# Kernel tuning notes

Measured on AMD Instinct MI355X. Metric: run time of the kernel, lower is better.

Reference implementation:

```python
import jax, jax.numpy as jnp
import numpy as np

N, E, F_IN, E_DIM, H, G = 8192, 40960, 32, 8, 64, 64
EPS = 1e-5


def _lin(key, fan_in, fan_out):
    k1, k2 = jax.random.split(key)
    s = 1.0 / np.sqrt(fan_in)
    w = jax.random.uniform(k1, (fan_in, fan_out), jnp.float32, -s, s)
    b = jax.random.uniform(k2, (fan_out,), jnp.float32, -s, s)
    return w, b


def setup_inputs() -> dict:
    key = jax.random.key(0)
    ks = jax.random.split(key, 32)
    inp = {}
    inp['x'] = jax.random.normal(ks[0], (N, F_IN), jnp.float32)
    inp['edge_index'] = jax.random.randint(ks[1], (2, E), 0, N)
    inp['edge_attr'] = jax.random.normal(ks[2], (E, E_DIM), jnp.float32)
    inp['batch'] = jnp.sort(jax.random.randint(ks[3], (N,), 0, G))
    # NNConv 1 (F_IN -> H)
    inp['e1_w1'], inp['e1_b1'] = _lin(ks[4], E_DIM, H)
    inp['e1_w2'], inp['e1_b2'] = _lin(ks[5], H, F_IN * H)
    inp['root1_w'], inp['root1_b'] = _lin(ks[6], F_IN, H)
    inp['bn1_g'] = jnp.ones((H,), jnp.float32); inp['bn1_b'] = jnp.zeros((H,), jnp.float32)
    # NNConv 2 (H -> H)
    inp['e2_w1'], inp['e2_b1'] = _lin(ks[7], E_DIM, H)
    inp['e2_w2'], inp['e2_b2'] = _lin(ks[8], H, H * H)
    inp['root2_w'], inp['root2_b'] = _lin(ks[9], H, H)
    inp['bn2_g'] = jnp.ones((H,), jnp.float32); inp['bn2_b'] = jnp.zeros((H,), jnp.float32)
    # NNConv 3 (H -> H)
    inp['e3_w1'], inp['e3_b1'] = _lin(ks[10], E_DIM, H)
    inp['e3_w2'], inp['e3_b2'] = _lin(ks[11], H, H * H)
    inp['root3_w'], inp['root3_b'] = _lin(ks[12], H, H)
    inp['bn3_g'] = jnp.ones((H,), jnp.float32); inp['bn3_b'] = jnp.zeros((H,), jnp.float32)
    # attention gate MLP: H -> H//2 -> 1
    inp['gate_w1'], inp['gate_b1'] = _lin(ks[13], H, H // 2)
    inp['gate_w2'], inp['gate_b2'] = _lin(ks[14], H // 2, 1)
    # fc head: H -> 2H (BN, relu) -> H (BN, relu) -> 1
    inp['fc1_w'], inp['fc1_b'] = _lin(ks[15], H, 2 * H)
    inp['fcbn1_g'] = jnp.ones((2 * H,), jnp.float32); inp['fcbn1_b'] = jnp.zeros((2 * H,), jnp.float32)
    inp['fc2_w'], inp['fc2_b'] = _lin(ks[16], 2 * H, H)
    inp['fcbn2_g'] = jnp.ones((H,), jnp.float32); inp['fcbn2_b'] = jnp.zeros((H,), jnp.float32)
    inp['fc3_w'], inp['fc3_b'] = _lin(ks[17], H, 1)
    return inp


def _bn(x, g, b):
    # training-mode batch norm over node/graph dim
    m = jnp.mean(x, axis=0)
    v = jnp.var(x, axis=0)
    return (x - m) * jax.lax.rsqrt(v + EPS) * g + b


def _nnconv(x, edge_index, edge_attr, w1, b1, w2, b2, root_w, root_b, in_ch, out_ch):
    src, dst = edge_index[0], edge_index[1]
    h = jax.nn.relu(edge_attr @ w1 + b1)                     # [E, H]
    We = (h @ w2 + b2).reshape(-1, in_ch, out_ch)            # [E, in, out]
    msg = jnp.einsum('ei,eio->eo', x[src], We)               # [E, out]
    s = jax.ops.segment_sum(msg, dst, num_segments=N)
    cnt = jax.ops.segment_sum(jnp.ones((msg.shape[0],), x.dtype), dst, num_segments=N)
    agg = s / jnp.clip(cnt, 1.0)[:, None]                    # mean aggregation
    return agg + x @ root_w + root_b


def _global_attention(x, batch, gw1, gb1, gw2, gb2):
    gate = jax.nn.relu(x @ gw1 + gb1) @ gw2 + gb2            # [N, 1]
    gate = gate[:, 0]
    m = jax.ops.segment_max(gate, batch, num_segments=G)
    e = jnp.exp(gate - m[batch])
    z = jax.ops.segment_sum(e, batch, num_segments=G)
    alpha = e / z[batch]
    return jax.ops.segment_sum(alpha[:, None] * x, batch, num_segments=G)  # [G, H]


def reference(x, edge_index, edge_attr, batch,
              e1_w1, e1_b1, e1_w2, e1_b2, root1_w, root1_b, bn1_g, bn1_b,
              e2_w1, e2_b1, e2_w2, e2_b2, root2_w, root2_b, bn2_g, bn2_b,
              e3_w1, e3_b1, e3_w2, e3_b2, root3_w, root3_b, bn3_g, bn3_b,
              gate_w1, gate_b1, gate_w2, gate_b2,
              fc1_w, fc1_b, fcbn1_g, fcbn1_b, fc2_w, fc2_b, fcbn2_g, fcbn2_b, fc3_w, fc3_b):
    x1 = jax.nn.relu(_bn(_nnconv(x, edge_index, edge_attr, e1_w1, e1_b1, e1_w2, e1_b2, root1_w, root1_b, F_IN, H), bn1_g, bn1_b))
    x2 = jax.nn.relu(_bn(_nnconv(x1, edge_index, edge_attr, e2_w1, e2_b1, e2_w2, e2_b2, root2_w, root2_b, H, H), bn2_g, bn2_b)) + x1
    x3 = jax.nn.relu(_bn(_nnconv(x2, edge_index, edge_attr, e3_w1, e3_b1, e3_w2, e3_b2, root3_w, root3_b, H, H), bn3_g, bn3_b)) + x2
    # dropout is identity in eval/reference mode
    p = _global_attention(x3, batch, gate_w1, gate_b1, gate_w2, gate_b2)  # [G, H]
    h = jax.nn.relu(_bn(p @ fc1_w + fc1_b, fcbn1_g, fcbn1_b))
    h = jax.nn.relu(_bn(h @ fc2_w + fc2_b, fcbn2_g, fcbn2_b))
    out = h @ fc3_w + fc3_b
    return out[:, 0]
```

## Files before the change

kernel.cpp:

```cpp
#include <hip/hip_runtime.h>
#include <hip/hip_bf16.h>

#define NN 8192
#define EE 40960
#define FIN 32
#define HH 64
#define GG 64

typedef __attribute__((ext_vector_type(4))) float f32x4;
typedef __attribute__((ext_vector_type(8))) short s16x8;
typedef unsigned short ushort_t;

__device__ __forceinline__ unsigned short f2bf(float f) {
    union { float f; unsigned int u; } v; v.f = f;
    unsigned int u = v.u;
    return (unsigned short)((u + 0x7fffu + ((u >> 16) & 1u)) >> 16);
}

__device__ __forceinline__ void gll16(const void* g, void* l) {
    __builtin_amdgcn_global_load_lds((__attribute__((address_space(1))) void*)g,
                                     (__attribute__((address_space(3))) void*)l, 16, 0, 0);
}

__global__ void btbuild_all_kernel(const float* __restrict__ w2a, const float* __restrict__ b2a, ushort_t* __restrict__ Bta,
                                   const float* __restrict__ w2b, const float* __restrict__ b2b, ushort_t* __restrict__ Btb,
                                   const float* __restrict__ w2c, const float* __restrict__ b2c, ushort_t* __restrict__ Btc,
                                   int* __restrict__ cnt, int* __restrict__ fill, float* __restrict__ stats) {
    int bid = blockIdx.x;
    int t = threadIdx.x;
    if (bid < 32) { cnt[bid * 256 + t] = 0; fill[bid * 256 + t] = 0; }
    if (bid == 32) stats[t] = 0.f;
    if (bid == 33 && t < 128) stats[256 + t] = 0.f;

    const float* w2; const float* b2; ushort_t* Bt; int IC; int base;
    if (bid < 520)       { w2 = w2a; b2 = b2a; Bt = Bta; IC = 32; base = bid; }
    else if (bid < 1560) { w2 = w2b; b2 = b2b; Bt = Btb; IC = 64; base = bid - 520; }
    else                 { w2 = w2c; b2 = b2c; Bt = Btc; IC = 64; base = bid - 1560; }
    int CH = IC >> 3;
    int flat = base * 256 + t;
    if (flat >= 64 * 65 * IC) return;
    int s = flat / (64 * IC);
    int rem = flat - s * (64 * IC);
    int row = rem / IC;
    int j = rem - row * IC;
    int q = j >> 3, w = j & 7;
    int c = q ^ (row & (CH - 1));
    int i = c * 8 + w;
    float v = (s < 64) ? w2[s * (IC * 64) + i * 64 + row] : b2[i * 64 + row];
    Bt[flat] = f2bf(v);
}

__global__ void hist_kernel(const int* __restrict__ dst, int* __restrict__ cnt) {
    int e = blockIdx.x * 256 + threadIdx.x;
    if (e < EE) atomicAdd(&cnt[dst[e]], 1);
}

__global__ void scan_kernel(const int* __restrict__ cnt, int* __restrict__ row_ptr) {
    __shared__ int lds[1024];
    int t = threadIdx.x;
    int v[8]; int s = 0;
    int base = t * 8;
#pragma unroll
    for (int j = 0; j < 8; j++) { v[j] = s; s += cnt[base + j]; }
    lds[t] = s;
    __syncthreads();
    for (int off = 1; off < 1024; off <<= 1) {
        int add = (t >= off) ? lds[t - off] : 0;
        __syncthreads();
        lds[t] += add;
        __syncthreads();
    }
    int ex = lds[t] - s;
#pragma unroll
    for (int j = 0; j < 8; j++) row_ptr[base + j] = ex + v[j];
    if (t == 1023) row_ptr[NN] = lds[1023];
}

__global__ void scatter_kernel(const int* __restrict__ dst, const int* __restrict__ row_ptr,
                               int* __restrict__ fill, int* __restrict__ perm) {
    int e = blockIdx.x * 256 + threadIdx.x;
    if (e < EE) {
        int d = dst[e];
        int pos = row_ptr[d] + atomicAdd(&fill[d], 1);
        perm[pos] = e;
    }
}

template<int IC>
__launch_bounds__(256, 5)
__global__ void conv_msg_kernel(const float* __restrict__ eattr,
                                const float* __restrict__ w1,
                                const float* __restrict__ b1,
                                const float* __restrict__ xin,
                                const int* __restrict__ src,
                                const int* __restrict__ perm,
                                const ushort_t* __restrict__ Bt,
                                float* __restrict__ msg) {
    constexpr int NKK  = IC / 32;
    constexpr int CH   = IC / 8;
    constexpr int TILE = IC * 64;
    constexpr int NQ   = (TILE * 2) / 4096;
    __shared__ ushort_t bt_lds[2][TILE];
    __shared__ float h_t[2048];
    __shared__ float ea_s[32][9];
    __shared__ float w1s[512];
    __shared__ float b1s[64];
    __shared__ int eid_s[32];

    const int t = threadIdx.x;
    const int wave = t >> 6;
    const int l = t & 63;
    const int g = l >> 4;
    const int rlo = l & 15;
    const int e0 = blockIdx.x * 32;

    auto stage = [&](int buf, int step) {
#pragma unroll
        for (int q = 0; q < NQ; ++q) {
            int off = q * 2048 + wave * 512;
            const ushort_t* gp = Bt + (size_t)step * TILE + off + l * 8;
            gll16(gp, &bt_lds[buf][off]);
        }
    };

    stage(0, 0);

    if (t < 32) eid_s[t] = perm[e0 + t];
    if (t < 64) b1s[t] = b1[t];
    for (int i = t; i < 512; i += 256) w1s[i] = w1[i];
    __syncthreads();

    { int e = t >> 3, i = t & 7; ea_s[e][i] = eattr[(size_t)eid_s[e] * 8 + i]; }

    s16x8 afrag[2][NKK];
#pragma unroll
    for (int m = 0; m < 2; ++m) {
        int row = m * 16 + rlo;
        int sn = src[eid_s[row]];
        const float* xp = xin + (size_t)sn * IC + g * 8;
#pragma unroll
        for (int kk = 0; kk < NKK; ++kk) {
            f32x4 a = *(const f32x4*)(xp + kk * 32);
            f32x4 b = *(const f32x4*)(xp + kk * 32 + 4);
            s16x8 fr;
            fr[0] = (short)f2bf(a[0]); fr[1] = (short)f2bf(a[1]);
            fr[2] = (short)f2bf(a[2]); fr[3] = (short)f2bf(a[3]);
            fr[4] = (short)f2bf(b[0]); fr[5] = (short)f2bf(b[1]);
            fr[6] = (short)f2bf(b[2]); fr[7] = (short)f2bf(b[3]);
            afrag[m][kk] = fr;
        }
    }
    __syncthreads();

#pragma unroll
    for (int j = 0; j < 8; ++j) {
        int idx = t + 256 * j;
        int k = idx >> 5, e = idx & 31;
        float s = b1s[k];
#pragma unroll
        for (int i = 0; i < 8; i++) s += ea_s[e][i] * w1s[i * 64 + k];
        h_t[idx] = fmaxf(s, 0.f);
    }
    __syncthreads();

    f32x4 acc[2];
#pragma unroll
    for (int m = 0; m < 2; m++) acc[m] = (f32x4){0.f, 0.f, 0.f, 0.f};

    const int bcol = wave * 16 + rlo;
    const int bmask = bcol & (CH - 1);
    const f32x4 zf = (f32x4){0.f, 0.f, 0.f, 0.f};

    for (int step = 0; step < 65; ++step) {
        if (step < 64) stage((step + 1) & 1, step + 1);
        const int buf = step & 1;
        s16x8 bfr[NKK];
#pragma unroll
        for (int kk = 0; kk < NKK; kk++) {
            int q = (kk * 4 + g) ^ bmask;
            bfr[kk] = *(const s16x8*)&bt_lds[buf][bcol * IC + q * 8];
        }
#pragma unroll
        for (int m = 0; m < 2; m++) {
            f32x4 P = __builtin_amdgcn_mfma_f32_16x16x32_bf16(afrag[m][0], bfr[0], zf, 0, 0, 0);
            if constexpr (NKK == 2)
                P = __builtin_amdgcn_mfma_f32_16x16x32_bf16(afrag[m][1], bfr[1], P, 0, 0, 0);
            if (step == 64) {
                acc[m] += P;
            } else {
                f32x4 h4 = *(const f32x4*)&h_t[(step << 5) + m * 16 + (g << 2)];
                acc[m] += h4 * P;
            }
        }
        __syncthreads();
    }

#pragma unroll
    for (int m = 0; m < 2; m++) {
        int row = e0 + m * 16 + (g << 2);
        float* mp = msg + (size_t)row * 64 + wave * 16 + rlo;
        mp[0] = acc[m][0]; mp[64] = acc[m][1]; mp[128] = acc[m][2]; mp[192] = acc[m][3];
    }
}

__global__ void aggregate_kernel(const float* __restrict__ msg, const int* __restrict__ row_ptr,
                                 const float* __restrict__ xin, int IC,
                                 const float* __restrict__ root_w, const float* __restrict__ root_b,
                                 float* __restrict__ y, float* __restrict__ stats) {
    int t = threadIdx.x;
    int n = blockIdx.x * 16 + (t >> 4);
    int cg = (t & 15) * 4;
    int s = row_ptr[n], e = row_ptr[n + 1];
    f32x4 acc = (f32x4){0.f, 0.f, 0.f, 0.f};
    for (int j = s; j < e; ++j) {
        acc += *(const f32x4*)&msg[(size_t)j * 64 + cg];
    }
    float inv = 1.0f / fmaxf((float)(e - s), 1.0f);
    acc *= inv;
    const float* xr = xin + (size_t)n * IC;
    for (int i = 0; i < IC; ++i) {
        float xv = xr[i];
        acc += xv * (*(const f32x4*)&root_w[i * 64 + cg]);
    }
    acc += *(const f32x4*)&root_b[cg];
    *(f32x4*)&y[(size_t)n * 64 + cg] = acc;

    f32x4 a2 = acc * acc;
#pragma unroll
    for (int j = 0; j < 4; j++) {
        acc[j] += __shfl_xor(acc[j], 16); acc[j] += __shfl_xor(acc[j], 32);
        a2[j]  += __shfl_xor(a2[j], 16);  a2[j]  += __shfl_xor(a2[j], 32);
    }
    __shared__ float ls[4][64], lq[4][64];
    int w = t >> 6;
    if ((t & 63) < 16) {
#pragma unroll
        for (int j = 0; j < 4; j++) { ls[w][cg + j] = acc[j]; lq[w][cg + j] = a2[j]; }
    }
    __syncthreads();
    if (t < 64) {
        float S = ls[0][t] + ls[1][t] + ls[2][t] + ls[3][t];
        float Q = lq[0][t] + lq[1][t] + lq[2][t] + lq[3][t];
        atomicAdd(&stats[t], S);
        atomicAdd(&stats[64 + t], Q);
    }
}

__global__ void bn_apply_kernel(const float* __restrict__ y, const float* __restrict__ stats,
                                const float* __restrict__ gam, const float* __restrict__ bet,
                                const float* __restrict__ res, float* __restrict__ xout) {
    int i4 = blockIdx.x * 256 + threadIdx.x;
    int cg = (i4 & 15) * 4;
    const float invN = 1.0f / (float)NN;
    f32x4 yv = *(const f32x4*)&y[(size_t)i4 * 4];
    f32x4 o;
#pragma unroll
    for (int j = 0; j < 4; j++) {
        int c = cg + j;
        float mean = stats[c] * invN;
        float var = stats[64 + c] * invN - mean * mean;
        float sc = rsqrtf(var + 1e-5f) * gam[c];
        float v = (yv[j] - mean) * sc + bet[c];
        o[j] = fmaxf(v, 0.f);
    }
    if (res) o += *(const f32x4*)&res[(size_t)i4 * 4];
    *(f32x4*)&xout[(size_t)i4 * 4] = o;
}

__global__ void bn_gate_kernel(const float* __restrict__ y, const float* __restrict__ stats,
                               const float* __restrict__ gam, const float* __restrict__ bet,
                               const float* __restrict__ res, float* __restrict__ xout,
                               const float* __restrict__ gw1, const float* __restrict__ gb1,
                               const float* __restrict__ gw2, const float* __restrict__ gb2,
                               float* __restrict__ gate) {
    __shared__ float x3s[64][68];
    __shared__ float w1s[2048];
    __shared__ float b1s[32], w2s[32];
    __shared__ float b2s;
    int t = threadIdx.x;
    for (int i = t; i < 2048; i += 256) w1s[i] = gw1[i];
    if (t < 32) { b1s[t] = gb1[t]; w2s[t] = gw2[t]; }
    if (t == 0) b2s = gb2[0];
    const float invN = 1.0f / (float)NN;
    size_t base4 = (size_t)blockIdx.x * 1024;
#pragma unroll
    for (int j = 0; j < 4; j++) {
        int i4l = j * 256 + t;
        int row = i4l >> 4, cg = (i4l & 15) * 4;
        f32x4 yv = *(const f32x4*)&y[(base4 + i4l) * 4];
        f32x4 o;
#pragma unroll
        for (int jj = 0; jj < 4; jj++) {
            int c = cg + jj;
            float mean = stats[c] * invN;
            float var = stats[64 + c] * invN - mean * mean;
            float sc = rsqrtf(var + 1e-5f) * gam[c];
            o[jj] = fmaxf((yv[jj] - mean) * sc + bet[c], 0.f);
        }
        o += *(const f32x4*)&res[(base4 + i4l) * 4];
        *(f32x4*)&xout[(base4 + i4l) * 4] = o;
        *(f32x4*)&x3s[row][cg] = o;
    }
    __syncthreads();
    int w = t >> 6, l = t & 63;
    int row = w * 16 + (l >> 2), part = l & 3;
    float hacc[8];
#pragma unroll
    for (int j = 0; j < 8; j++) hacc[j] = b1s[part * 8 + j];
    for (int i = 0; i < 64; i++) {
        float xv = x3s[row][i];
#pragma unroll
        for (int j = 0; j < 8; j++) hacc[j] += xv * w1s[i * 32 + part * 8 + j];
    }
    float gv = 0.f;
#pragma unroll
    for (int j = 0; j < 8; j++) gv += fmaxf(hacc[j], 0.f) * w2s[part * 8 + j];
    gv += __shfl_xor(gv, 1); gv += __shfl_xor(gv, 2);
    if (part == 0) gate[blockIdx.x * 64 + row] = gv + b2s;
}

__global__ void attn_pool_kernel(const float* __restrict__ x3, const float* __restrict__ gate,
                                 const int* __restrict__ batch, float* __restrict__ p) {
    int g = blockIdx.x;
    int t = threadIdx.x;
    int lo = 0, hi = NN;
    while (lo < hi) { int mid = (lo + hi) >> 1; if (batch[mid] < g) lo = mid + 1; else hi = mid; }
    int s = lo;
    hi = NN;
    while (lo < hi) { int mid = (lo + hi) >> 1; if (batch[mid] < g + 1) lo = mid + 1; else hi = mid; }
    int e = lo;

    __shared__ float red[4];
    __shared__ float sM, sZ;
    float m = -1e30f;
    for (int n = s + t; n < e; n += 256) m = fmaxf(m, gate[n]);
#pragma unroll
    for (int off = 1; off < 64; off <<= 1) m = fmaxf(m, __shfl_xor(m, off));
    if ((t & 63) == 0) red[t >> 6] = m;
    __syncthreads();
    if (t == 0) sM = fmaxf(fmaxf(red[0], red[1]), fmaxf(red[2], red[3]));
    __syncthreads();
    float z = 0.f;
    for (int n = s + t; n < e; n += 256) z += __expf(gate[n] - sM);
#pragma unroll
    for (int off = 1; off < 64; off <<= 1) z += __shfl_xor(z, off);
    if ((t & 63) == 0) red[t >> 6] = z;
    __syncthreads();
    if (t == 0) sZ = red[0] + red[1] + red[2] + red[3];
    __syncthreads();
    int w = t >> 6, c = t & 63;
    float acc = 0.f;
    for (int n = s + w; n < e; n += 4) acc += __expf(gate[n] - sM) * x3[(size_t)n * 64 + c];
    __shared__ float pa[4][64];
    pa[w][c] = acc;
    __syncthreads();
    if (t < 64) {
        float v = pa[0][t] + pa[1][t] + pa[2][t] + pa[3][t];
        p[g * 64 + t] = (sZ > 0.f) ? v / sZ : 0.f;
    }
}

__global__ void head1_kernel(const float* __restrict__ p, const float* __restrict__ fc1w,
                             const float* __restrict__ fc1b, const float* __restrict__ bn1g,
                             const float* __restrict__ bn1b, float* __restrict__ t1n) {
    __shared__ float sp[64 * 65];
    __shared__ float w1s[64 * 16];
    __shared__ float t1s[64 * 17];
    __shared__ float sA[16], sB[16];
    int t = threadIdx.x;
    int c0 = blockIdx.x * 16;
    for (int i = t; i < 4096; i += 256) { int r = i >> 6, cc = i & 63; sp[r * 65 + cc] = p[i]; }
    for (int i = t; i < 1024; i += 256) { int r = i >> 4, cc = i & 15; w1s[i] = fc1w[r * 128 + c0 + cc]; }
    __syncthreads();
    int r16 = t >> 4, c = t & 15;
    float b = fc1b[c0 + c];
#pragma unroll
    for (int rb = 0; rb < 4; rb++) {
        int row = rb * 16 + r16;
        float s = b;
#pragma unroll 8
        for (int i = 0; i < 64; i++) s += sp[row * 65 + i] * w1s[i * 16 + c];
        t1s[row * 17 + c] = s;
    }
    __syncthreads();
    if (t < 16) {
        float su = 0.f, sq = 0.f;
        for (int r = 0; r < 64; r++) { float v = t1s[r * 17 + t]; su += v; sq += v * v; }
        float mean = su * (1.f / 64.f), var = sq * (1.f / 64.f) - mean * mean;
        float sc = rsqrtf(var + 1e-5f) * bn1g[c0 + t];
        sA[t] = sc; sB[t] = bn1b[c0 + t] - mean * sc;
    }
    __syncthreads();
#pragma unroll
    for (int rb = 0; rb < 4; rb++) {
        int row = rb * 16 + r16;
        float v = t1s[row * 17 + c] * sA[c] + sB[c];
        t1n[row * 128 + c0 + c] = fmaxf(v, 0.f);
    }
}

__global__ void head2_kernel(const float* __restrict__ t1n, const float* __restrict__ fc2w,
                             const float* __restrict__ fc2b, const float* __restrict__ bn2g,
                             const float* __restrict__ bn2b, float* __restrict__ y2n) {
    __shared__ float t1sh[64 * 129];
    __shared__ float w2s[128 * 8];
    __shared__ float t2s[64 * 9];
    __shared__ float sA[8], sB[8];
    int t = threadIdx.x;
    int c0 = blockIdx.x * 8;
    for (int i = t; i < 8192; i += 256) { int r = i >> 7, cc = i & 127; t1sh[r * 129 + cc] = t1n[i]; }
    for (int i = t; i < 1024; i += 256) { int r = i >> 3, cc = i & 7; w2s[i] = fc2w[r * 64 + c0 + cc]; }
    __syncthreads();
    int r32 = t >> 3, c = t & 7;
    float b = fc2b[c0 + c];
#pragma unroll
    for (int rb = 0; rb < 2; rb++) {
        int row = rb * 32 + r32;
        float s = b;
#pragma unroll 8
        for (int i = 0; i < 128; i++) s += t1sh[row * 129 + i] * w2s[i * 8 + c];
        t2s[row * 9 + c] = s;
    }
    __syncthreads();
    if (t < 8) {
        float su = 0.f, sq = 0.f;
        for (int r = 0; r < 64; r++) { float v = t2s[r * 9 + t]; su += v; sq += v * v; }
        float mean = su * (1.f / 64.f), var = sq * (1.f / 64.f) - mean * mean;
        float sc = rsqrtf(var + 1e-5f) * bn2g[c0 + t];
        sA[t] = sc; sB[t] = bn2b[c0 + t] - mean * sc;
    }
    __syncthreads();
#pragma unroll
    for (int rb = 0; rb < 2; rb++) {
        int row = rb * 32 + r32;
        float v = t2s[row * 9 + c] * sA[c] + sB[c];
        y2n[row * 64 + c0 + c] = fmaxf(v, 0.f);
    }
}

__global__ void head3_kernel(const float* __restrict__ y2n, const float* __restrict__ fc3w,
                             const float* __restrict__ fc3b, float* __restrict__ out) {
    __shared__ float w3[64];
    int t = threadIdx.x;
    w3[t] = fc3w[t];
    __syncthreads();
    float s = fc3b[0];
    const float* yr = y2n + t * 64;
#pragma unroll 8
    for (int i = 0; i < 64; i++) s += yr[i] * w3[i];
    out[t] = s;
}

extern "C" void kernel_launch(void* const* d_in, const int* in_sizes, int n_in,
                              void* d_out, int out_size, void* d_ws, size_t ws_size,
                              hipStream_t stream) {
    const float* x     = (const float*)d_in[0];
    const int*   eidx  = (const int*)d_in[1];
    const float* eattr = (const float*)d_in[2];
    const int*   batch = (const int*)d_in[3];
    const float* e1w1 = (const float*)d_in[4];  const float* e1b1 = (const float*)d_in[5];
    const float* e1w2 = (const float*)d_in[6];  const float* e1b2 = (const float*)d_in[7];
    const float* r1w  = (const float*)d_in[8];  const float* r1b  = (const float*)d_in[9];
    const float* bn1g = (const float*)d_in[10]; const float* bn1b = (const float*)d_in[11];
    const float* e2w1 = (const float*)d_in[12]; const float* e2b1 = (const float*)d_in[13];
    const float* e2w2 = (const float*)d_in[14]; const float* e2b2 = (const float*)d_in[15];
    const float* r2w  = (const float*)d_in[16]; const float* r2b  = (const float*)d_in[17];
    const float* bn2g = (const float*)d_in[18]; const float* bn2b = (const float*)d_in[19];
    const float* e3w1 = (const float*)d_in[20]; const float* e3b1 = (const float*)d_in[21];
    const float* e3w2 = (const float*)d_in[22]; const float* e3b2 = (const float*)d_in[23];
    const float* r3w  = (const float*)d_in[24]; const float* r3b  = (const float*)d_in[25];
    const float* bn3g = (const float*)d_in[26]; const float* bn3b = (const float*)d_in[27];
    const float* gw1  = (const float*)d_in[28]; const float* gb1  = (const float*)d_in[29];
    const float* gw2  = (const float*)d_in[30]; const float* gb2  = (const float*)d_in[31];
    const float* fc1w = (const float*)d_in[32]; const float* fc1b = (const float*)d_in[33];
    const float* fbn1g= (const float*)d_in[34]; const float* fbn1b= (const float*)d_in[35];
    const float* fc2w = (const float*)d_in[36]; const float* fc2b = (const float*)d_in[37];
    const float* fbn2g= (const float*)d_in[38]; const float* fbn2b= (const float*)d_in[39];
    const float* fc3w = (const float*)d_in[40]; const float* fc3b = (const float*)d_in[41];
    float* out = (float*)d_out;

    const int* src = eidx;
    const int* dst = eidx + EE;

    char* ws = (char*)d_ws;
    size_t off = 0;
    auto take = [&](size_t n) { void* p = ws + off; off = (off + n + 255) & ~(size_t)255; return p; };
    ushort_t* Bt1 = (ushort_t*)take((size_t)65 * 2048 * 2);
    ushort_t* Bt2 = (ushort_t*)take((size_t)65 * 4096 * 2);
    ushort_t* Bt3 = (ushort_t*)take((size_t)65 * 4096 * 2);
    float* msg  = (float*)take((size_t)EE * 64 * 4);
    float* ybuf = (float*)take((size_t)NN * 64 * 4);
    float* x1   = (float*)take((size_t)NN * 64 * 4);
    float* x2   = (float*)take((size_t)NN * 64 * 4);
    float* x3   = (float*)take((size_t)NN * 64 * 4);
    float* gate = (float*)take((size_t)NN * 4);
    float* pbuf = (float*)take(64 * 64 * 4);
    float* t1n  = (float*)take(64 * 128 * 4);
    float* y2n  = (float*)take(64 * 64 * 4);
    float* stats = (float*)take(384 * 4);
    int* cnt  = (int*)take((size_t)NN * 4);
    int* fill = (int*)take((size_t)NN * 4);
    int* rowp = (int*)take((size_t)(NN + 1) * 4);
    int* perm = (int*)take((size_t)EE * 4);

    btbuild_all_kernel<<<2600, 256, 0, stream>>>(e1w2, e1b2, Bt1, e2w2, e2b2, Bt2,
                                                 e3w2, e3b2, Bt3, cnt, fill, stats);
    hist_kernel<<<160, 256, 0, stream>>>(dst, cnt);
    scan_kernel<<<1, 1024, 0, stream>>>(cnt, rowp);
    scatter_kernel<<<160, 256, 0, stream>>>(dst, rowp, fill, perm);

    conv_msg_kernel<32><<<1280, 256, 0, stream>>>(eattr, e1w1, e1b1, x, src, perm, Bt1, msg);
    aggregate_kernel<<<512, 256, 0, stream>>>(msg, rowp, x, 32, r1w, r1b, ybuf, stats);
    bn_apply_kernel<<<512, 256, 0, stream>>>(ybuf, stats, bn1g, bn1b, nullptr, x1);

    conv_msg_kernel<64><<<1280, 256, 0, stream>>>(eattr, e2w1, e2b1, x1, src, perm, Bt2, msg);
    aggregate_kernel<<<512, 256, 0, stream>>>(msg, rowp, x1, 64, r2w, r2b, ybuf, stats + 128);
    bn_apply_kernel<<<512, 256, 0, stream>>>(ybuf, stats + 128, bn2g, bn2b, x1, x2);

    conv_msg_kernel<64><<<1280, 256, 0, stream>>>(eattr, e3w1, e3b1, x2, src, perm, Bt3, msg);
    aggregate_kernel<<<512, 256, 0, stream>>>(msg, rowp, x2, 64, r3w, r3b, ybuf, stats + 256);
    bn_gate_kernel<<<128, 256, 0, stream>>>(ybuf, stats + 256, bn3g, bn3b, x2, x3,
                                            gw1, gb1, gw2, gb2, gate);

    attn_pool_kernel<<<64, 256, 0, stream>>>(x3, gate, batch, pbuf);
    head1_kernel<<<8, 256, 0, stream>>>(pbuf, fc1w, fc1b, fbn1g, fbn1b, t1n);
    head2_kernel<<<8, 256, 0, stream>>>(t1n, fc2w, fc2b, fbn2g, fbn2b, y2n);
    head3_kernel<<<1, 64, 0, stream>>>(y2n, fc3w, fc3b, out);
}
```

Before: 261.7 us.

## Precompute root linear transform in producer kernels and read it during aggregation

Moves the per-node root linear (x @ root_w + root_b) out of the aggregate kernel. For layer 1 the extra blocks appended to the btbuild launch compute it; for layers 2 and 3 the bn_apply kernel computes it from the freshly normalized activations using shared-memory staged weights. Aggregation then only adds a precomputed row. This removes the per-thread global weight-row loop from aggregation, at the cost of an extra NN x 64 buffer round-trip and a larger shared-memory footprint in bn_apply.

```diff
diff --git a/kernel.cpp b/kernel.cpp
--- a/kernel.cpp
+++ b/kernel.cpp
@@ -25,9 +25,32 @@
 __global__ void btbuild_all_kernel(const float* __restrict__ w2a, const float* __restrict__ b2a, ushort_t* __restrict__ Bta,
                                    const float* __restrict__ w2b, const float* __restrict__ b2b, ushort_t* __restrict__ Btb,
                                    const float* __restrict__ w2c, const float* __restrict__ b2c, ushort_t* __restrict__ Btc,
-                                   int* __restrict__ cnt, int* __restrict__ fill, float* __restrict__ stats) {
+                                   int* __restrict__ cnt, int* __restrict__ fill, float* __restrict__ stats,
+                                   const float* __restrict__ x, const float* __restrict__ r1w,
+                                   const float* __restrict__ r1b, float* __restrict__ rootbuf) {
     int bid = blockIdx.x;
     int t = threadIdx.x;
+
+    if (bid >= 2600) {
+        __shared__ float xs[16][36];
+        __shared__ float rws[32 * 64];
+        __shared__ float rbs[64];
+        int blk = bid - 2600;
+        for (int j = t; j < 512; j += 256) { int r = j >> 5, i = j & 31; xs[r][i] = x[(size_t)(blk * 16 + r) * 32 + i]; }
+        for (int i = t; i < 2048; i += 256) rws[i] = r1w[i];
+        if (t < 64) rbs[t] = r1b[t];
+        __syncthreads();
+        int r = t >> 4, cg = (t & 15) * 4;
+        f32x4 s = *(const f32x4*)&rbs[cg];
+#pragma unroll 8
+        for (int i = 0; i < 32; i++) {
+            float xv = xs[r][i];
+            s += xv * (*(const f32x4*)&rws[i * 64 + cg]);
+        }
+        *(f32x4*)&rootbuf[(size_t)(blk * 16 + r) * 64 + cg] = s;
+        return;
+    }
+
     if (bid < 32) { cnt[bid * 256 + t] = 0; fill[bid * 256 + t] = 0; }
     if (bid == 32) stats[t] = 0.f;
     if (bid == 33 && t < 128) stats[256 + t] = 0.f;
@@ -204,8 +227,7 @@
 }
 
 __global__ void aggregate_kernel(const float* __restrict__ msg, const int* __restrict__ row_ptr,
-                                 const float* __restrict__ xin, int IC,
-                                 const float* __restrict__ root_w, const float* __restrict__ root_b,
+                                 const float* __restrict__ rootbuf,
                                  float* __restrict__ y, float* __restrict__ stats) {
     int t = threadIdx.x;
     int n = blockIdx.x * 16 + (t >> 4);
@@ -217,12 +239,7 @@
     }
     float inv = 1.0f / fmaxf((float)(e - s), 1.0f);
     acc *= inv;
-    const float* xr = xin + (size_t)n * IC;
-    for (int i = 0; i < IC; ++i) {
-        float xv = xr[i];
-        acc += xv * (*(const f32x4*)&root_w[i * 64 + cg]);
-    }
-    acc += *(const f32x4*)&root_b[cg];
+    acc += *(const f32x4*)&rootbuf[(size_t)n * 64 + cg];
     *(f32x4*)&y[(size_t)n * 64 + cg] = acc;
 
     f32x4 a2 = acc * acc;
@@ -246,11 +263,19 @@
     }
 }
 
-__global__ void bn_apply_kernel(const float* __restrict__ y, const float* __restrict__ stats,
-                                const float* __restrict__ gam, const float* __restrict__ bet,
-                                const float* __restrict__ res, float* __restrict__ xout) {
-    int i4 = blockIdx.x * 256 + threadIdx.x;
-    int cg = (i4 & 15) * 4;
+__global__ void bn_apply_root_kernel(const float* __restrict__ y, const float* __restrict__ stats,
+                                     const float* __restrict__ gam, const float* __restrict__ bet,
+                                     const float* __restrict__ res, float* __restrict__ xout,
+                                     const float* __restrict__ rw, const float* __restrict__ rb,
+                                     float* __restrict__ rootbuf) {
+    __shared__ float xs[16][68];
+    __shared__ float rws[64 * 64];
+    __shared__ float rbs[64];
+    int t = threadIdx.x;
+    for (int i = t; i < 4096; i += 256) rws[i] = rw[i];
+    if (t < 64) rbs[t] = rb[t];
+    int i4 = blockIdx.x * 256 + t;
+    int row = t >> 4, cg = (t & 15) * 4;
     const float invN = 1.0f / (float)NN;
     f32x4 yv = *(const f32x4*)&y[(size_t)i4 * 4];
     f32x4 o;
@@ -260,11 +285,19 @@
         float mean = stats[c] * invN;
         float var = stats[64 + c] * invN - mean * mean;
         float sc = rsqrtf(var + 1e-5f) * gam[c];
-        float v = (yv[j] - mean) * sc + bet[c];
-        o[j] = fmaxf(v, 0.f);
+        o[j] = fmaxf((yv[j] - mean) * sc + bet[c], 0.f);
     }
     if (res) o += *(const f32x4*)&res[(size_t)i4 * 4];
     *(f32x4*)&xout[(size_t)i4 * 4] = o;
+    *(f32x4*)&xs[row][cg] = o;
+    __syncthreads();
+    f32x4 s = *(const f32x4*)&rbs[cg];
+#pragma unroll 8
+    for (int i = 0; i < 64; i++) {
+        float xv = xs[row][i];
+        s += xv * (*(const f32x4*)&rws[i * 64 + cg]);
+    }
+    *(f32x4*)&rootbuf[(size_t)(blockIdx.x * 16 + row) * 64 + cg] = s;
 }
 
 __global__ void bn_gate_kernel(const float* __restrict__ y, const float* __restrict__ stats,
@@ -493,6 +526,7 @@
     float* x1   = (float*)take((size_t)NN * 64 * 4);
     float* x2   = (float*)take((size_t)NN * 64 * 4);
     float* x3   = (float*)take((size_t)NN * 64 * 4);
+    float* rootbuf = (float*)take((size_t)NN * 64 * 4);
     float* gate = (float*)take((size_t)NN * 4);
     float* pbuf = (float*)take(64 * 64 * 4);
     float* t1n  = (float*)take(64 * 128 * 4);
@@ -503,22 +537,25 @@
     int* rowp = (int*)take((size_t)(NN + 1) * 4);
     int* perm = (int*)take((size_t)EE * 4);
 
-    btbuild_all_kernel<<<2600, 256, 0, stream>>>(e1w2, e1b2, Bt1, e2w2, e2b2, Bt2,
-                                                 e3w2, e3b2, Bt3, cnt, fill, stats);
+    btbuild_all_kernel<<<3112, 256, 0, stream>>>(e1w2, e1b2, Bt1, e2w2, e2b2, Bt2,
+                                                 e3w2, e3b2, Bt3, cnt, fill, stats,
+                                                 x, r1w, r1b, rootbuf);
     hist_kernel<<<160, 256, 0, stream>>>(dst, cnt);
     scan_kernel<<<1, 1024, 0, stream>>>(cnt, rowp);
     scatter_kernel<<<160, 256, 0, stream>>>(dst, rowp, fill, perm);
 
     conv_msg_kernel<32><<<1280, 256, 0, stream>>>(eattr, e1w1, e1b1, x, src, perm, Bt1, msg);
-    aggregate_kernel<<<512, 256, 0, stream>>>(msg, rowp, x, 32, r1w, r1b, ybuf, stats);
-    bn_apply_kernel<<<512, 256, 0, stream>>>(ybuf, stats, bn1g, bn1b, nullptr, x1);
+    aggregate_kernel<<<512, 256, 0, stream>>>(msg, rowp, rootbuf, ybuf, stats);
+    bn_apply_root_kernel<<<512, 256, 0, stream>>>(ybuf, stats, bn1g, bn1b, nullptr, x1,
+                                                  r2w, r2b, rootbuf);
 
     conv_msg_kernel<64><<<1280, 256, 0, stream>>>(eattr, e2w1, e2b1, x1, src, perm, Bt2, msg);
-    aggregate_kernel<<<512, 256, 0, stream>>>(msg, rowp, x1, 64, r2w, r2b, ybuf, stats + 128);
-    bn_apply_kernel<<<512, 256, 0, stream>>>(ybuf, stats + 128, bn2g, bn2b, x1, x2);
+    aggregate_kernel<<<512, 256, 0, stream>>>(msg, rowp, rootbuf, ybuf, stats + 128);
+    bn_apply_root_kernel<<<512, 256, 0, stream>>>(ybuf, stats + 128, bn2g, bn2b, x1, x2,
+                                                  r3w, r3b, rootbuf);
 
     conv_msg_kernel<64><<<1280, 256, 0, stream>>>(eattr, e3w1, e3b1, x2, src, perm, Bt3, msg);
-    aggregate_kernel<<<512, 256, 0, stream>>>(msg, rowp, x2, 64, r3w, r3b, ybuf, stats + 256);
+    aggregate_kernel<<<512, 256, 0, stream>>>(msg, rowp, rootbuf, ybuf, stats + 256);
     bn_gate_kernel<<<128, 256, 0, stream>>>(ybuf, stats + 256, bn3g, bn3b, x2, x3,
                                             gw1, gb1, gw2, gb2, gate);
 
```

After: 239.3 us. 1.09x faster.
